# Performance work log

Hardware: AMD Instinct MI355X
Metric: run time of the kernel (lower is better)

## Reference

```python
import jax, jax.numpy as jnp
import numpy as np

N = 100000
NEG_SLOPE = 0.2
EPS = 1e-16


def _gat_layer(x, W, a_src, a_dst, b, src, dst, heads, dim, concat):
    # Linear projection -> [N, H, D]
    h = (x @ W).reshape(x.shape[0], heads, dim)
    # Per-node attention logits [N, H]
    al_src = jnp.sum(h * a_src[None], axis=-1)
    al_dst = jnp.sum(h * a_dst[None], axis=-1)
    # Per-edge logits, leaky relu (negative_slope=0.2)
    e = al_src[src] + al_dst[dst]                      # [E, H]
    e = jnp.where(e >= 0, e, NEG_SLOPE * e)
    # Scatter softmax over destination neighborhoods
    emax = jax.ops.segment_max(e, dst, num_segments=N)  # [N, H]
    ee = jnp.exp(e - emax[dst])
    denom = jax.ops.segment_sum(ee, dst, num_segments=N)
    alpha = ee / (denom[dst] + EPS)                    # [E, H]
    # Weighted scatter-add aggregation
    msg = h[src] * alpha[:, :, None]                   # [E, H, D]
    out = jax.ops.segment_sum(msg, dst, num_segments=N)  # [N, H, D]
    if concat:
        out = out.reshape(N, heads * dim)
    else:
        out = out.mean(axis=1)
    return out + b


def setup_inputs() -> dict:
    key = jax.random.key(0)
    ks = jax.random.split(key, 10)
    F_in, hid, H, C = 500, 8, 8, 3
    E = 3200000
    x = jax.random.normal(ks[0], (N, F_in), dtype=jnp.float32)
    edge_index = jax.random.randint(ks[1], (2, E), 0, N, dtype=jnp.int64)
    s1 = (1.0 / np.sqrt(F_in)).astype(np.float32)
    s2 = (1.0 / np.sqrt(hid * H)).astype(np.float32)
    return {
        "x": x,
        "edge_index": edge_index,
        "W1": jax.random.normal(ks[2], (F_in, H * hid), dtype=jnp.float32) * s1,
        "att_src1": jax.random.normal(ks[3], (H, hid), dtype=jnp.float32),
        "att_dst1": jax.random.normal(ks[4], (H, hid), dtype=jnp.float32),
        "b1": jnp.zeros((H * hid,), dtype=jnp.float32),
        "W2": jax.random.normal(ks[5], (H * hid, C), dtype=jnp.float32) * s2,
        "att_src2": jax.random.normal(ks[6], (1, C), dtype=jnp.float32),
        "att_dst2": jax.random.normal(ks[7], (1, C), dtype=jnp.float32),
        "b2": jnp.zeros((C,), dtype=jnp.float32),
    }


def reference(x, edge_index, W1, att_src1, att_dst1, b1, W2, att_src2, att_dst2, b2):
    # Add self-loops (PyG GATConv default)
    loop = jnp.arange(N, dtype=edge_index.dtype)
    src = jnp.concatenate([edge_index[0], loop])
    dst = jnp.concatenate([edge_index[1], loop])
    # Layer 1: 8 heads, concat -> [N, 64], ELU
    h = _gat_layer(x, W1, att_src1, att_dst1, b1, src, dst, heads=8, dim=8, concat=True)
    h = jax.nn.elu(h)
    # Layer 2: 1 head, no concat -> [N, 3]
    out = _gat_layer(h, W2, att_src2, att_dst2, b2, src, dst, heads=1, dim=3, concat=False)
    return out, jax.nn.log_softmax(out, axis=1)
```

## Files before the change

### kernel.cpp

```cpp
#include <hip/hip_runtime.h>
#include <hip/hip_bf16.h>


#define F_IN 500
#define HEADS 8
#define HID 8
#define HD 64
#define CLS 3
#define NEG 0.2f
#define EPSV 1e-16f
#define LOG2E 1.44269504088896340736f

#define NBLK_H 256
#define NBKT_MAX 3136

typedef __attribute__((ext_vector_type(8))) short short8v;
typedef __attribute__((ext_vector_type(4))) float f32x4;

__device__ inline short bfs(float v) {
    __hip_bfloat16 b = __float2bfloat16(v);
    return *(short*)&b;
}

__device__ inline int ld_edge(const void* ei, long idx, int is64) {
    return is64 ? (int)((const long long*)ei)[idx] : ((const int*)ei)[idx];
}

__global__ void k_prepW(const float* __restrict__ W1, ushort* __restrict__ W1b2,
                        const int* __restrict__ ei, int* __restrict__ flag) {
    if (blockIdx.x == 0 && threadIdx.x == 0) {
        int z = 0;
        for (int i = 1; i < 16; i += 2) z += (ei[i] == 0) ? 1 : 0;
        *flag = (z == 8) ? 1 : 0;
    }
    int i = blockIdx.x * 256 + threadIdx.x;
    if (i >= 16 * 64 * 32) return;
    int ks = i >> 11;
    int c = (i >> 5) & 63;
    int st = i & 31;
    int q = (st >> 3) ^ ((c >> 1) & 3);
    int k = ks * 32 + q * 8 + (st & 7);
    float v = (k < F_IN) ? W1[k * HD + c] : 0.f;
    __hip_bfloat16 b = __float2bfloat16(v);
    W1b2[i] = *(ushort*)&b;
}

__device__ __forceinline__ void g1_stage(const float* __restrict__ x,
        const ushort* __restrict__ W1b2, char* smem, int buf, int ks,
        int rowb, int N, int lane, int w) {
    const int k0 = ks * 32;
    {
        const ushort* srcB = W1b2 + ks * 2048 + (w * 64 + lane) * 8;
        char* dstB = smem + 16384 + buf * 4096 + w * 1024;
        __builtin_amdgcn_global_load_lds(
            (const __attribute__((address_space(1))) void*)srcB,
            (__attribute__((address_space(3))) void*)dstB, 16, 0, 0);
    }
#pragma unroll
    for (int i = 0; i < 2; ++i) {
        int vt = i * 256 + w * 64 + lane;
        int row = vt >> 3;
        int c = (vt & 7) ^ (row & 7);
        int ke = k0 + c * 4; if (ke > 496) ke = 496;
        int rowg = rowb + row; if (rowg >= N) rowg = N - 1;
        const float* srcA = x + (long)rowg * F_IN + ke;
        char* dstA = smem + buf * 8192 + i * 4096 + w * 1024;
        __builtin_amdgcn_global_load_lds(
            (const __attribute__((address_space(1))) void*)srcA,
            (__attribute__((address_space(3))) void*)dstA, 16, 0, 0);
    }
}

__global__ __launch_bounds__(256) void k_fatA(const float* __restrict__ x,
        const ushort* __restrict__ W1b2,
        const float* __restrict__ asrc, const float* __restrict__ adst,
        float* __restrict__ als, float* __restrict__ ald,
        ushort* __restrict__ h1b, int N,
        const void* ei, int E, int nbkt, int* __restrict__ ghist,
        const int* __restrict__ flag) {
    __shared__ char smem[24576];
    int gB = (N + 63) >> 6;
    int t = threadIdx.x;

    if ((int)blockIdx.x >= gB) {
        int hb = blockIdx.x - gB;
        int* h = (int*)smem;
        int tot = E + N;
        int epb = (tot + NBLK_H - 1) / NBLK_H;
        int e0 = hb * epb, e1 = min(tot, e0 + epb);
        for (int i = t; i < nbkt; i += 256) h[i] = 0;
        __syncthreads();
        int is64 = *flag;
        for (int e = e0 + t; e < e1; e += 256) {
            int dst = (e < E) ? ld_edge(ei, (long)E + e, is64) : (e - E);
            atomicAdd(&h[dst >> 5], 1);
        }
        __syncthreads();
        for (int i = t; i < nbkt; i += 256)
            ghist[hb * nbkt + i] = h[i];
        return;
    }

    int lane = t & 63;
    int w = t >> 6;
    int l16 = lane & 15, oct = lane >> 4;
    int rowb = blockIdx.x * 64;

    f32x4 acc0 = {0.f, 0.f, 0.f, 0.f};
    f32x4 acc1 = {0.f, 0.f, 0.f, 0.f};
    f32x4 acc2 = {0.f, 0.f, 0.f, 0.f};
    f32x4 acc3 = {0.f, 0.f, 0.f, 0.f};

    g1_stage(x, W1b2, smem, 0, 0, rowb, N, lane, w);
    __syncthreads();

    int rl = w * 16 + l16;
    int asw = l16 & 7;
    int bsw = (l16 >> 1) & 3;

    for (int ks = 0; ks < 16; ++ks) {
        int cur = ks & 1;
        if (ks < 15)
            g1_stage(x, W1b2, smem, cur ^ 1, ks + 1, rowb, N, lane, w);
        const char* Ab = smem + cur * 8192;
        const char* Bb = smem + 16384 + cur * 4096;
        float4 x0 = *reinterpret_cast<const float4*>(
            Ab + rl * 128 + ((2 * oct + 0) ^ asw) * 16);
        float4 x1 = *reinterpret_cast<const float4*>(
            Ab + rl * 128 + ((2 * oct + 1) ^ asw) * 16);
        short8v a;
        a[0] = bfs(x0.x); a[1] = bfs(x0.y); a[2] = bfs(x0.z); a[3] = bfs(x0.w);
        a[4] = bfs(x1.x); a[5] = bfs(x1.y); a[6] = bfs(x1.z); a[7] = bfs(x1.w);
        short8v b0 = *reinterpret_cast<const short8v*>(
            Bb + (0 * 16 + l16) * 64 + (oct ^ bsw) * 16);
        short8v b1 = *reinterpret_cast<const short8v*>(
            Bb + (1 * 16 + l16) * 64 + (oct ^ bsw) * 16);
        short8v b2 = *reinterpret_cast<const short8v*>(
            Bb + (2 * 16 + l16) * 64 + (oct ^ bsw) * 16);
        short8v b3 = *reinterpret_cast<const short8v*>(
            Bb + (3 * 16 + l16) * 64 + (oct ^ bsw) * 16);
        acc0 = __builtin_amdgcn_mfma_f32_16x16x32_bf16(a, b0, acc0, 0, 0, 0);
        acc1 = __builtin_amdgcn_mfma_f32_16x16x32_bf16(a, b1, acc1, 0, 0, 0);
        acc2 = __builtin_amdgcn_mfma_f32_16x16x32_bf16(a, b2, acc2, 0, 0, 0);
        acc3 = __builtin_amdgcn_mfma_f32_16x16x32_bf16(a, b3, acc3, 0, 0, 0);
        __syncthreads();
    }

    float* fs = (float*)smem;
#pragma unroll
    for (int r = 0; r < 4; ++r) {
        int rl_ = w * 16 + oct * 4 + r;
        fs[rl_ * 64 + l16 +  0] = acc0[r];
        fs[rl_ * 64 + l16 + 16] = acc1[r];
        fs[rl_ * 64 + l16 + 32] = acc2[r];
        fs[rl_ * 64 + l16 + 48] = acc3[r];
    }
    __syncthreads();
#pragma unroll
    for (int j = t; j < 512; j += 256) {
        int row = j >> 3, h = j & 7;
        int gn = rowb + row;
        if (gn < N) {
            const float* hp = fs + row * 64 + h * 8;
            float4 v0 = *reinterpret_cast<const float4*>(hp);
            float4 v1 = *reinterpret_cast<const float4*>(hp + 4);
            const float* s = asrc + h * 8;
            const float* d = adst + h * 8;
            float s1 = v0.x * s[0] + v0.y * s[1] + v0.z * s[2] + v0.w * s[3]
                     + v1.x * s[4] + v1.y * s[5] + v1.z * s[6] + v1.w * s[7];
            float s2 = v0.x * d[0] + v0.y * d[1] + v0.z * d[2] + v0.w * d[3]
                     + v1.x * d[4] + v1.y * d[5] + v1.z * d[6] + v1.w * d[7];
            als[gn * 8 + h] = s1 * LOG2E;
            ald[gn * 8 + h] = s2 * LOG2E;
            ushort hb[8];
            hb[0] = (ushort)bfs(v0.x); hb[1] = (ushort)bfs(v0.y);
            hb[2] = (ushort)bfs(v0.z); hb[3] = (ushort)bfs(v0.w);
            hb[4] = (ushort)bfs(v1.x); hb[5] = (ushort)bfs(v1.y);
            hb[6] = (ushort)bfs(v1.z); hb[7] = (ushort)bfs(v1.w);
            *reinterpret_cast<uint4*>(h1b + (long)gn * HD + h * 8) =
                *reinterpret_cast<const uint4*>(hb);
        }
    }
}


__global__ void k_bsum(const int* __restrict__ ghist, int* __restrict__ colsum, int nbkt) {
    int b = blockIdx.x * 256 + threadIdx.x;
    if (b >= nbkt) return;
    int s = 0;
    for (int i = 0; i < NBLK_H; i++) s += ghist[i * nbkt + b];
    colsum[b] = s;
}

__global__ __launch_bounds__(256) void k_bscan2(const int* __restrict__ colsum,
        int* __restrict__ boff, int nbkt) {
    __shared__ int part[256];
    int per = (nbkt + 255) / 256;
    int t = threadIdx.x;
    int lo = t * per, hi = min(nbkt, lo + per);
    int s = 0;
    for (int i = lo; i < hi; i++) s += colsum[i];
    part[t] = s;
    __syncthreads();
    for (int off = 1; off < 256; off <<= 1) {
        int v = (t >= off) ? part[t - off] : 0;
        __syncthreads();
        part[t] += v;
        __syncthreads();
    }
    int run = (t > 0) ? part[t - 1] : 0;
    for (int i = lo; i < hi; i++) { boff[i] = run; run += colsum[i]; }
    if (t == 255) boff[nbkt] = part[255];
}

__global__ void k_bapply(int* __restrict__ ghist, const int* __restrict__ boff, int nbkt) {
    int b = blockIdx.x * 256 + threadIdx.x;
    if (b >= nbkt) return;
    int run = boff[b];
    for (int i = 0; i < NBLK_H; i++) {
        int v = ghist[i * nbkt + b];
        ghist[i * nbkt + b] = run;
        run += v;
    }
}

__global__ __launch_bounds__(256) void k_scatter(const void* ei, int E, int N, int nbkt,
        const int* __restrict__ ghist, uint* __restrict__ pairs, const int* flag) {
    __shared__ int cur[NBKT_MAX];
    int tot = E + N;
    int epb = (tot + NBLK_H - 1) / NBLK_H;
    int e0 = blockIdx.x * epb, e1 = min(tot, e0 + epb);
    for (int i = threadIdx.x; i < nbkt; i += 256) cur[i] = ghist[blockIdx.x * nbkt + i];
    __syncthreads();
    int is64 = *flag;
    for (int e = e0 + threadIdx.x; e < e1; e += 256) {
        int src, dst;
        if (e < E) { src = ld_edge(ei, e, is64); dst = ld_edge(ei, (long)E + e, is64); }
        else { src = dst = e - E; }
        int pos = atomicAdd(&cur[dst >> 5], 1);
        pairs[pos] = ((uint)src << 5) | (uint)(dst & 31);
    }
}

__global__ __launch_bounds__(256) void k_fill3(const uint* __restrict__ pairs,
        const int* __restrict__ boff, int* __restrict__ rowptr,
        int* __restrict__ csr, int N, int nbkt) {
    __shared__ int cnt[32];
    __shared__ int base[32];
    __shared__ int cur[32];
    int b = blockIdx.x;
    int t = threadIdx.x;
    if (t < 32) { cnt[t] = 0; cur[t] = 0; }
    __syncthreads();
    int p0 = boff[b], p1 = boff[b + 1];
    for (int p = p0 + t; p < p1; p += 256)
        atomicAdd(&cnt[pairs[p] & 31], 1);
    __syncthreads();
    if (t < 32) {
        int pre = 0;
#pragma unroll
        for (int i = 0; i < 32; i++) pre += (i < t) ? cnt[i] : 0;
        base[t] = p0 + pre;
        int n = b * 32 + t;
        if (n < N) rowptr[n] = base[t];
    }
    if (b == 0 && t == 0) rowptr[N] = boff[nbkt];
    __syncthreads();
    for (int p = p0 + t; p < p1; p += 256) {
        uint v = pairs[p];
        int lo = v & 31;
        int pos = base[lo] + atomicAdd(&cur[lo], 1);
        csr[pos] = (int)(v >> 5);
    }
}

__global__ __launch_bounds__(256) void k_agg1(const int* __restrict__ rowptr,
        const int* __restrict__ csr, const ushort* __restrict__ h1b,
        const float* __restrict__ als, const float* __restrict__ ald,
        const float* __restrict__ b1, const float* __restrict__ W2,
        const float* __restrict__ as2, const float* __restrict__ ad2,
        float* __restrict__ h2p, float* __restrict__ ald2, int N) {
    int lane = threadIdx.x & 63;
    int wid = threadIdx.x >> 6;
    int half = lane >> 5;
    int n = blockIdx.x * 8 + wid * 2 + half;
    bool act = (n < N);
    int nc = act ? n : (N - 1);
    int es = (lane >> 3) & 3;
    int h = lane & 7;
    float aldh = ald[nc * HEADS + h];
    int rs = rowptr[nc], re = rowptr[nc + 1];

    float acc[4][8];
    float den[4] = {0.f, 0.f, 0.f, 0.f};
#pragma unroll
    for (int q = 0; q < 4; ++q)
#pragma unroll
        for (int j = 0; j < 8; ++j) acc[q][j] = 0.f;

    int jb = rs;
    for (; jb + 16 <= re; jb += 16) {
        int s[4]; float e[4]; float p[4]; uint4 u[4];
#pragma unroll
        for (int q = 0; q < 4; ++q) s[q] = csr[jb + q * 4 + es];
#pragma unroll
        for (int q = 0; q < 4; ++q) {
            e[q] = als[s[q] * HEADS + h] + aldh;
            u[q] = *reinterpret_cast<const uint4*>(h1b + (long)s[q] * HD + h * 8);
        }
#pragma unroll
        for (int q = 0; q < 4; ++q) {
            e[q] = fmaxf(e[q], NEG * e[q]);
            p[q] = exp2f(e[q]);
        }
#pragma unroll
        for (int q = 0; q < 4; ++q) {
            acc[q][0] += p[q] * __uint_as_float(u[q].x << 16);
            acc[q][1] += p[q] * __uint_as_float(u[q].x & 0xffff0000u);
            acc[q][2] += p[q] * __uint_as_float(u[q].y << 16);
            acc[q][3] += p[q] * __uint_as_float(u[q].y & 0xffff0000u);
            acc[q][4] += p[q] * __uint_as_float(u[q].z << 16);
            acc[q][5] += p[q] * __uint_as_float(u[q].z & 0xffff0000u);
            acc[q][6] += p[q] * __uint_as_float(u[q].w << 16);
            acc[q][7] += p[q] * __uint_as_float(u[q].w & 0xffff0000u);
            den[q] += p[q];
        }
    }
    for (; jb < re; jb += 4) {
        int eidx = jb + es;
        bool valid = (eidx < re);
        int s = csr[valid ? eidx : rs];
        float e = als[s * HEADS + h] + aldh;
        e = fmaxf(e, NEG * e);
        float p = valid ? exp2f(e) : 0.f;
        uint4 u = *reinterpret_cast<const uint4*>(h1b + (long)s * HD + h * 8);
        acc[0][0] += p * __uint_as_float(u.x << 16);
        acc[0][1] += p * __uint_as_float(u.x & 0xffff0000u);
        acc[0][2] += p * __uint_as_float(u.y << 16);
        acc[0][3] += p * __uint_as_float(u.y & 0xffff0000u);
        acc[0][4] += p * __uint_as_float(u.z << 16);
        acc[0][5] += p * __uint_as_float(u.z & 0xffff0000u);
        acc[0][6] += p * __uint_as_float(u.w << 16);
        acc[0][7] += p * __uint_as_float(u.w & 0xffff0000u);
        den[0] += p;
    }
    float a0 = (acc[0][0] + acc[1][0]) + (acc[2][0] + acc[3][0]);
    float a1 = (acc[0][1] + acc[1][1]) + (acc[2][1] + acc[3][1]);
    float a2 = (acc[0][2] + acc[1][2]) + (acc[2][2] + acc[3][2]);
    float a3 = (acc[0][3] + acc[1][3]) + (acc[2][3] + acc[3][3]);
    float a4 = (acc[0][4] + acc[1][4]) + (acc[2][4] + acc[3][4]);
    float a5 = (acc[0][5] + acc[1][5]) + (acc[2][5] + acc[3][5]);
    float a6 = (acc[0][6] + acc[1][6]) + (acc[2][6] + acc[3][6]);
    float a7 = (acc[0][7] + acc[1][7]) + (acc[2][7] + acc[3][7]);
    float dn = (den[0] + den[1]) + (den[2] + den[3]);
#pragma unroll
    for (int off = 8; off <= 16; off <<= 1) {
        dn += __shfl_xor(dn, off);
        a0 += __shfl_xor(a0, off); a1 += __shfl_xor(a1, off);
        a2 += __shfl_xor(a2, off); a3 += __shfl_xor(a3, off);
        a4 += __shfl_xor(a4, off); a5 += __shfl_xor(a5, off);
        a6 += __shfl_xor(a6, off); a7 += __shfl_xor(a7, off);
    }
    float sel_a = (es < 2) ? ((es == 0) ? a0 : a1) : ((es == 2) ? a2 : a3);
    float sel_b = (es < 2) ? ((es == 0) ? a4 : a5) : ((es == 2) ? a6 : a7);
    int da = h * 8 + es, db = da + 4;
    float inv = 1.f / (dn + EPSV);
    float oa = sel_a * inv + b1[da];
    float ob = sel_b * inv + b1[db];
    oa = (oa > 0.f) ? oa : __expf(oa) - 1.f;
    ob = (ob > 0.f) ? ob : __expf(ob) - 1.f;
    float p0 = oa * W2[da * CLS + 0] + ob * W2[db * CLS + 0];
    float p1 = oa * W2[da * CLS + 1] + ob * W2[db * CLS + 1];
    float p2 = oa * W2[da * CLS + 2] + ob * W2[db * CLS + 2];
#pragma unroll
    for (int off = 1; off <= 16; off <<= 1) {
        p0 += __shfl_xor(p0, off);
        p1 += __shfl_xor(p1, off);
        p2 += __shfl_xor(p2, off);
    }
    if ((lane & 31) == 0 && act) {
        float als2v = (p0 * as2[0] + p1 * as2[1] + p2 * as2[2]) * LOG2E;
        *reinterpret_cast<float4*>(h2p + (long)n * 4) =
            make_float4(p0, p1, p2, als2v);
        ald2[n] = (p0 * ad2[0] + p1 * ad2[1] + p2 * ad2[2]) * LOG2E;
    }
}

__global__ __launch_bounds__(256) void k_agg2(const int* __restrict__ rowptr,
        const int* __restrict__ csr, const float* __restrict__ h2p,
        const float* __restrict__ ald2v,
        const float* __restrict__ b2, float* __restrict__ out, int N) {
    int n = blockIdx.x * 8 + (threadIdx.x >> 5);
    if (n >= N) return;
    int lane = threadIdx.x & 31;
    float aldv = ald2v[n];
    int rs = rowptr[n], re = rowptr[n + 1];
    float sum = 0.f, a0 = 0.f, a1 = 0.f, a2 = 0.f;
    for (int j = rs + lane; j < re; j += 32) {
        int s = csr[j];
        float4 hv = *reinterpret_cast<const float4*>(h2p + (long)s * 4);
        float e = hv.w + aldv;
        e = fmaxf(e, NEG * e);
        float p = exp2f(e);
        sum += p;
        a0 += p * hv.x;
        a1 += p * hv.y;
        a2 += p * hv.z;
    }
#pragma unroll
    for (int off = 1; off < 32; off <<= 1) {
        sum += __shfl_xor(sum, off);
        a0 += __shfl_xor(a0, off);
        a1 += __shfl_xor(a1, off);
        a2 += __shfl_xor(a2, off);
    }
    if (lane == 0) {
        float d = sum + EPSV;
        float v0 = a0 / d + b2[0], v1 = a1 / d + b2[1], v2 = a2 / d + b2[2];
        float mx = fmaxf(v0, fmaxf(v1, v2));
        float se = __expf(v0 - mx) + __expf(v1 - mx) + __expf(v2 - mx);
        float ls = mx + __logf(se);
        out[n * CLS + 0] = v0; out[n * CLS + 1] = v1; out[n * CLS + 2] = v2;
        long o2 = (long)N * CLS;
        out[o2 + n * CLS + 0] = v0 - ls;
        out[o2 + n * CLS + 1] = v1 - ls;
        out[o2 + n * CLS + 2] = v2 - ls;
    }
}

extern "C" void kernel_launch(void* const* d_in, const int* in_sizes, int n_in,
                              void* d_out, int out_size, void* d_ws, size_t ws_size,
                              hipStream_t stream) {
    const float* x   = (const float*)d_in[0];
    const void*  ei  = d_in[1];
    const float* W1  = (const float*)d_in[2];
    const float* as1 = (const float*)d_in[3];
    const float* ad1 = (const float*)d_in[4];
    const float* b1  = (const float*)d_in[5];
    const float* W2  = (const float*)d_in[6];
    const float* as2 = (const float*)d_in[7];
    const float* ad2 = (const float*)d_in[8];
    const float* b2  = (const float*)d_in[9];
    int N = in_sizes[0] / F_IN;
    int E = in_sizes[1] / 2;
    int tot = E + N;
    int nbkt = (N + 31) >> 5;

    char* w = (char*)d_ws;
    auto alloc = [&](size_t bytes) -> char* {
        char* p = w; w += (bytes + 255) & ~size_t(255); return p;
    };
    ushort* h1b    = (ushort*)alloc((size_t)N * HD * 2);
    float*  als1   = (float*)alloc((size_t)N * HEADS * 4);
    float*  ald1   = (float*)alloc((size_t)N * HEADS * 4);
    int*    rowptr = (int*)alloc((size_t)(N + 1) * 4);
    int*    csr    = (int*)alloc((size_t)tot * 4);
    float*  h2p    = (float*)alloc((size_t)N * 4 * 4);
    float*  ald2   = (float*)alloc((size_t)N * 4);
    ushort* W1b2   = (ushort*)alloc((size_t)16 * 64 * 32 * 2);
    int*    flag   = (int*)alloc(256);
    uint*   pairs  = (uint*)alloc((size_t)tot * 4);
    int*    ghist  = (int*)alloc((size_t)NBLK_H * nbkt * 4);
    int*    colsum = (int*)alloc((size_t)nbkt * 4);
    int*    boff   = (int*)alloc((size_t)(nbkt + 1) * 4);

    int gB = (N + 63) / 64;
    k_prepW<<<(16 * 64 * 32 + 255) / 256, 256, 0, stream>>>(W1, W1b2, (const int*)ei, flag);
    k_fatA<<<gB + NBLK_H, 256, 0, stream>>>(x, W1b2, as1, ad1, als1, ald1, h1b, N,
                                            ei, E, nbkt, ghist, flag);
    k_bsum<<<(nbkt + 255) / 256, 256, 0, stream>>>(ghist, colsum, nbkt);
    k_bscan2<<<1, 256, 0, stream>>>(colsum, boff, nbkt);
    k_bapply<<<(nbkt + 255) / 256, 256, 0, stream>>>(ghist, boff, nbkt);
    k_scatter<<<NBLK_H, 256, 0, stream>>>(ei, E, N, nbkt, ghist, pairs, flag);
    k_fill3<<<nbkt, 256, 0, stream>>>(pairs, boff, rowptr, csr, N, nbkt);
    k_agg1<<<(N + 7) / 8, 256, 0, stream>>>(rowptr, csr, h1b, als1, ald1, b1,
                                            W2, as2, ad2, h2p, ald2, N);
    k_agg2<<<(N + 7) / 8, 256, 0, stream>>>(rowptr, csr, h2p, ald2, b2,
                                            (float*)d_out, N);
}
```

Before: 285.1 us.

## Load full W1 into LDS once and stream x rows directly into registers

Replaces the double-buffered LDS staging of both x and W1 with a single up-front load of all of bf16 W1 into 64KB of LDS. Each lane now loads its own x row slices straight from global memory into registers with a 4-deep prefetch ring, which removes the per-k-step __syncthreads. The last partial K chunk is handled separately with bounds-checked scalar loads. The larger LDS footprint lowers occupancy, and the per-lane x loads are strided across rows rather than coalesced.

```diff
diff --git a/kernel.cpp b/kernel.cpp
--- a/kernel.cpp
+++ b/kernel.cpp
@@ -45,32 +45,6 @@
     W1b2[i] = *(ushort*)&b;
 }
 
-__device__ __forceinline__ void g1_stage(const float* __restrict__ x,
-        const ushort* __restrict__ W1b2, char* smem, int buf, int ks,
-        int rowb, int N, int lane, int w) {
-    const int k0 = ks * 32;
-    {
-        const ushort* srcB = W1b2 + ks * 2048 + (w * 64 + lane) * 8;
-        char* dstB = smem + 16384 + buf * 4096 + w * 1024;
-        __builtin_amdgcn_global_load_lds(
-            (const __attribute__((address_space(1))) void*)srcB,
-            (__attribute__((address_space(3))) void*)dstB, 16, 0, 0);
-    }
-#pragma unroll
-    for (int i = 0; i < 2; ++i) {
-        int vt = i * 256 + w * 64 + lane;
-        int row = vt >> 3;
-        int c = (vt & 7) ^ (row & 7);
-        int ke = k0 + c * 4; if (ke > 496) ke = 496;
-        int rowg = rowb + row; if (rowg >= N) rowg = N - 1;
-        const float* srcA = x + (long)rowg * F_IN + ke;
-        char* dstA = smem + buf * 8192 + i * 4096 + w * 1024;
-        __builtin_amdgcn_global_load_lds(
-            (const __attribute__((address_space(1))) void*)srcA,
-            (__attribute__((address_space(3))) void*)dstA, 16, 0, 0);
-    }
-}
-
 __global__ __launch_bounds__(256) void k_fatA(const float* __restrict__ x,
         const ushort* __restrict__ W1b2,
         const float* __restrict__ asrc, const float* __restrict__ adst,
@@ -78,7 +52,7 @@
         ushort* __restrict__ h1b, int N,
         const void* ei, int E, int nbkt, int* __restrict__ ghist,
         const int* __restrict__ flag) {
-    __shared__ char smem[24576];
+    __shared__ char smem[65536];
     int gB = (N + 63) >> 6;
     int t = threadIdx.x;
 
@@ -106,31 +80,47 @@
     int l16 = lane & 15, oct = lane >> 4;
     int rowb = blockIdx.x * 64;
 
+#pragma unroll
+    for (int i = 0; i < 16; ++i) {
+        const ushort* srcB = W1b2 + (size_t)(i * 256 + w * 64 + lane) * 8;
+        char* dstB = smem + (i * 256 + w * 64) * 16;
+        __builtin_amdgcn_global_load_lds(
+            (const __attribute__((address_space(1))) void*)srcB,
+            (__attribute__((address_space(3))) void*)dstB, 16, 0, 0);
+    }
+
+    int row = rowb + w * 16 + l16;
+    int rowc = (row < N) ? row : (N - 1);
+    const float* xr = x + (long)rowc * F_IN;
+    const float* xro = xr + oct * 8;
+
+    float4 pfa[4], pfb[4];
+#pragma unroll
+    for (int q = 0; q < 4; ++q) {
+        pfa[q] = *reinterpret_cast<const float4*>(xro + q * 32);
+        pfb[q] = *reinterpret_cast<const float4*>(xro + q * 32 + 4);
+    }
+
+    __syncthreads();
+
     f32x4 acc0 = {0.f, 0.f, 0.f, 0.f};
     f32x4 acc1 = {0.f, 0.f, 0.f, 0.f};
     f32x4 acc2 = {0.f, 0.f, 0.f, 0.f};
     f32x4 acc3 = {0.f, 0.f, 0.f, 0.f};
-
-    g1_stage(x, W1b2, smem, 0, 0, rowb, N, lane, w);
-    __syncthreads();
-
-    int rl = w * 16 + l16;
-    int asw = l16 & 7;
     int bsw = (l16 >> 1) & 3;
 
-    for (int ks = 0; ks < 16; ++ks) {
-        int cur = ks & 1;
-        if (ks < 15)
-            g1_stage(x, W1b2, smem, cur ^ 1, ks + 1, rowb, N, lane, w);
-        const char* Ab = smem + cur * 8192;
-        const char* Bb = smem + 16384 + cur * 4096;
-        float4 x0 = *reinterpret_cast<const float4*>(
-            Ab + rl * 128 + ((2 * oct + 0) ^ asw) * 16);
-        float4 x1 = *reinterpret_cast<const float4*>(
-            Ab + rl * 128 + ((2 * oct + 1) ^ asw) * 16);
+#pragma unroll
+    for (int ks = 0; ks < 15; ++ks) {
+        const int cur = ks & 3;
+        float4 x0 = pfa[cur], x1 = pfb[cur];
+        if (ks + 4 < 15) {
+            pfa[cur] = *reinterpret_cast<const float4*>(xro + (ks + 4) * 32);
+            pfb[cur] = *reinterpret_cast<const float4*>(xro + (ks + 4) * 32 + 4);
+        }
         short8v a;
         a[0] = bfs(x0.x); a[1] = bfs(x0.y); a[2] = bfs(x0.z); a[3] = bfs(x0.w);
         a[4] = bfs(x1.x); a[5] = bfs(x1.y); a[6] = bfs(x1.z); a[7] = bfs(x1.w);
+        const char* Bb = smem + ks * 4096;
         short8v b0 = *reinterpret_cast<const short8v*>(
             Bb + (0 * 16 + l16) * 64 + (oct ^ bsw) * 16);
         short8v b1 = *reinterpret_cast<const short8v*>(
@@ -143,9 +133,29 @@
         acc1 = __builtin_amdgcn_mfma_f32_16x16x32_bf16(a, b1, acc1, 0, 0, 0);
         acc2 = __builtin_amdgcn_mfma_f32_16x16x32_bf16(a, b2, acc2, 0, 0, 0);
         acc3 = __builtin_amdgcn_mfma_f32_16x16x32_bf16(a, b3, acc3, 0, 0, 0);
-        __syncthreads();
-    }
-
+    }
+    {
+        int kb = 480 + oct * 8;
+        short8v a;
+#pragma unroll
+        for (int j = 0; j < 8; ++j)
+            a[j] = bfs((kb + j < F_IN) ? xr[kb + j] : 0.f);
+        const char* Bb = smem + 15 * 4096;
+        short8v b0 = *reinterpret_cast<const short8v*>(
+            Bb + (0 * 16 + l16) * 64 + (oct ^ bsw) * 16);
+        short8v b1 = *reinterpret_cast<const short8v*>(
+            Bb + (1 * 16 + l16) * 64 + (oct ^ bsw) * 16);
+        short8v b2 = *reinterpret_cast<const short8v*>(
+            Bb + (2 * 16 + l16) * 64 + (oct ^ bsw) * 16);
+        short8v b3 = *reinterpret_cast<const short8v*>(
+            Bb + (3 * 16 + l16) * 64 + (oct ^ bsw) * 16);
+        acc0 = __builtin_amdgcn_mfma_f32_16x16x32_bf16(a, b0, acc0, 0, 0, 0);
+        acc1 = __builtin_amdgcn_mfma_f32_16x16x32_bf16(a, b1, acc1, 0, 0, 0);
+        acc2 = __builtin_amdgcn_mfma_f32_16x16x32_bf16(a, b2, acc2, 0, 0, 0);
+        acc3 = __builtin_amdgcn_mfma_f32_16x16x32_bf16(a, b3, acc3, 0, 0, 0);
+    }
+
+    __syncthreads();
     float* fs = (float*)smem;
 #pragma unroll
     for (int r = 0; r < 4; ++r) {
@@ -158,10 +168,10 @@
     __syncthreads();
 #pragma unroll
     for (int j = t; j < 512; j += 256) {
-        int row = j >> 3, h = j & 7;
-        int gn = rowb + row;
+        int rr = j >> 3, h = j & 7;
+        int gn = rowb + rr;
         if (gn < N) {
-            const float* hp = fs + row * 64 + h * 8;
+            const float* hp = fs + rr * 64 + h * 8;
             float4 v0 = *reinterpret_cast<const float4*>(hp);
             float4 v1 = *reinterpret_cast<const float4*>(hp + 4);
             const float* s = asrc + h * 8;
```

Result: slower. 300.2 us (+5.3%).
